# Kernel optimization log

Hardware: AMD Instinct MI355X
Metric: run time of the kernel (lower is better)

## Reference

```python
import jax, jax.numpy as jnp
import numpy as np

B, IN, N, OUT = 65536, 512, 256, 64  # batch, in_size, neurons, out_size


def setup_inputs() -> dict:
    key = jax.random.key(0)
    k1, k2, k3, k4 = jax.random.split(key, 4)
    return {
        "x": jax.random.normal(k1, (B, IN), jnp.float32),
        "W_lin": jax.random.normal(k2, (IN, N + OUT), jnp.float32),   # nlinear
        "W_nl": jax.random.normal(k3, (N - 1, N), jnp.float32),        # padded nonlinear[i] rows
        "W_out": jax.random.normal(k4, (OUT, N), jnp.float32),         # output_weights[0:out_size]
    }


def reference(x, W_lin, W_nl, W_out):
    act = jnp.tanh
    lin = x @ W_lin  # [B, N+OUT]
    # row i of nonlinear weights is valid only for entries 0..i (length i+1)
    tri_mask = (jnp.arange(N)[None, :] <= jnp.arange(N - 1)[:, None]).astype(lin.dtype)
    Wm = W_nl * tri_mask  # [N-1, N]
    # growing accumulator, fixed-size buffer; position 0 = lin[0] + 1
    acc0 = jnp.zeros((x.shape[0], N), lin.dtype).at[:, 0].set(lin[:, 0] + 1.0)
    col = jnp.arange(N)[None, :]

    def step(acc, inp):
        w, l, i = inp  # w: [N] masked weights, l: [B] = lin[:, i], i: scalar step
        v = jnp.sum(act(acc) * w[None, :], axis=1) + l + 1.0  # [B]
        acc = jnp.where(col == (i + 1), v[:, None], acc)
        return acc, None

    xs = (Wm, lin[:, : N - 1].T, jnp.arange(N - 1))
    acc, _ = jax.lax.scan(step, acc0, xs)
    # outs[i] = act(t) @ output_weights[i] + lin[neurons + i] + 1
    out = act(acc) @ W_out.T + lin[:, N:] + 1.0  # [B, OUT]
    return out
```

## Files before the change

### kernel.cpp

```cpp
#include <hip/hip_runtime.h>
#include <hip/hip_bf16.h>

typedef _Float16 f16x8 __attribute__((ext_vector_type(8)));
typedef unsigned short u16x8 __attribute__((ext_vector_type(8)));
typedef float f32x4 __attribute__((ext_vector_type(4)));
typedef unsigned int u32x4 __attribute__((ext_vector_type(4)));

static __device__ __forceinline__ unsigned short h2u(_Float16 h) {
    return __builtin_bit_cast(unsigned short, h);
}
static __device__ __forceinline__ float fast_tanh(float x) {
    float e = __expf(2.0f * x);
    return 1.0f - 2.0f / (e + 1.0f);
}

__global__ void cascade_prep(const float* __restrict__ W_lin,
                             const float* __restrict__ W_nl,
                             const float* __restrict__ W_out,
                             unsigned short* __restrict__ wlin_h,
                             unsigned short* __restrict__ wlin_l,
                             unsigned short* __restrict__ wnl_h,
                             unsigned short* __restrict__ wnl_l,
                             unsigned short* __restrict__ wout_h,
                             unsigned short* __restrict__ wout_l,
                             float* __restrict__ wcol) {
    int idx = blockIdx.x * blockDim.x + threadIdx.x;
    int stride = gridDim.x * blockDim.x;
    for (int i = idx; i < 320 * 512; i += stride) {
        int n = i >> 9, k = i & 511;
        float w = W_lin[k * 320 + n];
        _Float16 h = (_Float16)w;
        wlin_h[i] = h2u(h);
        wlin_l[i] = h2u((_Float16)(w - (float)h));
    }
    for (int i = idx; i < 255 * 256; i += stride) {
        int r = i >> 8, k = i & 255;
        float w = (k <= r) ? W_nl[i] : 0.0f;
        _Float16 h = (_Float16)w;
        wnl_h[i] = h2u(h);
        wnl_l[i] = h2u((_Float16)(w - (float)h));
    }
    for (int i = idx; i < 64 * 256; i += stride) {
        float w = W_out[i];
        _Float16 h = (_Float16)w;
        wout_h[i] = h2u(h);
        wout_l[i] = h2u((_Float16)(w - (float)h));
    }
    for (int i = idx; i < 256; i += stride) {
        int b = i >> 5, u = i & 31;
        float* dst = wcol + b * 496 + (31 * u - (u * (u - 1)) / 2);
        for (int j = u + 1; j < 32; ++j)
            dst[j - u - 1] = W_nl[(size_t)(b * 32 + j - 1) * 256 + b * 32 + u];
    }
}

__global__ __launch_bounds__(512, 1) void lin_gemm(
    const float* __restrict__ x,
    const unsigned short* __restrict__ wlin_h,
    const unsigned short* __restrict__ wlin_l,
    float* __restrict__ linc,
    float* __restrict__ lino) {

    __shared__ _Float16 bufH[2][16 * 520];
    __shared__ _Float16 bufL[2][16 * 520];

    const int tid = threadIdx.x;
    const int wv  = tid >> 6;
    const int l15 = tid & 15;
    const int g   = (tid & 63) >> 4;
    const int s = (blockIdx.x & 7) * 64 + (blockIdx.x >> 3);
    const long row0 = (long)s * 128;

    f16x8 xfh[16], xfl[16];
    {
        const float* xp = x + (row0 + wv * 16 + l15) * 512 + g * 8;
        #pragma unroll
        for (int ks = 0; ks < 16; ++ks) {
            float4 p0 = *reinterpret_cast<const float4*>(xp + ks * 32);
            float4 p1 = *reinterpret_cast<const float4*>(xp + ks * 32 + 4);
            float av[8] = {p0.x, p0.y, p0.z, p0.w, p1.x, p1.y, p1.z, p1.w};
            f16x8 fh, fl;
            #pragma unroll
            for (int e = 0; e < 8; ++e) {
                _Float16 hh = (_Float16)av[e];
                fh[e] = hh;
                fl[e] = (_Float16)(av[e] - (float)hh);
            }
            xfh[ks] = fh;
            xfl[ks] = fl;
        }
    }

    u16x8 rh[2], rl[2];
    #define STAGE_LOAD(nt)                                                     \
        {                                                                      \
            _Pragma("unroll")                                                  \
            for (int it = 0; it < 2; ++it) {                                   \
                int flat = it * 4096 + tid * 8;                                \
                int r = flat >> 9, c = flat & 511;                             \
                rh[it] = *reinterpret_cast<const u16x8*>(                      \
                    wlin_h + (size_t)((nt) * 16 + r) * 512 + c);               \
                rl[it] = *reinterpret_cast<const u16x8*>(                      \
                    wlin_l + (size_t)((nt) * 16 + r) * 512 + c);               \
            }                                                                  \
        }
    #define STAGE_WRITE(buf)                                                   \
        {                                                                      \
            _Pragma("unroll")                                                  \
            for (int it = 0; it < 2; ++it) {                                   \
                int flat = it * 4096 + tid * 8;                                \
                int r = flat >> 9, c = flat & 511;                             \
                *reinterpret_cast<u16x8*>(&bufH[buf][r * 520 + c]) =           \
                    __builtin_bit_cast(u16x8, rh[it]);                         \
                *reinterpret_cast<u16x8*>(&bufL[buf][r * 520 + c]) =           \
                    __builtin_bit_cast(u16x8, rl[it]);                         \
            }                                                                  \
        }

    STAGE_LOAD(0);
    STAGE_WRITE(0);
    __syncthreads();

    int cur = 0;
    for (int nt = 0; nt < 20; ++nt) {
        if (nt < 19) STAGE_LOAD(nt + 1);

        f32x4 acc = (f32x4){0.f, 0.f, 0.f, 0.f};
        if (nt < 16) {
            #pragma unroll
            for (int ks = 0; ks < 16; ++ks) {
                f16x8 bh = *reinterpret_cast<const f16x8*>(
                    &bufH[cur][l15 * 520 + ks * 32 + g * 8]);
                f16x8 bl = *reinterpret_cast<const f16x8*>(
                    &bufL[cur][l15 * 520 + ks * 32 + g * 8]);
                acc = __builtin_amdgcn_mfma_f32_16x16x32_f16(xfh[ks], bh, acc, 0, 0, 0);
                acc = __builtin_amdgcn_mfma_f32_16x16x32_f16(xfl[ks], bh, acc, 0, 0, 0);
                acc = __builtin_amdgcn_mfma_f32_16x16x32_f16(xfh[ks], bl, acc, 0, 0, 0);
            }
            int c = nt * 16 + l15;
            #pragma unroll
            for (int j = 0; j < 4; ++j) {
                long row = row0 + wv * 16 + g * 4 + j;
                if (c < 255) linc[row * 256 + c + 1] = acc[j];
                if (c == 0)  linc[row * 256] = acc[j];
            }
        } else {
            #pragma unroll
            for (int ks = 0; ks < 16; ++ks) {
                f16x8 bh = *reinterpret_cast<const f16x8*>(
                    &bufH[cur][l15 * 520 + ks * 32 + g * 8]);
                acc = __builtin_amdgcn_mfma_f32_16x16x32_f16(xfh[ks], bh, acc, 0, 0, 0);
            }
            #pragma unroll
            for (int j = 0; j < 4; ++j)
                lino[(row0 + wv * 16 + g * 4 + j) * 64 + (nt - 16) * 16 + l15] = acc[j];
        }

        if (nt < 19) STAGE_WRITE(cur ^ 1);
        __syncthreads();
        cur ^= 1;
    }
    #undef STAGE_LOAD
    #undef STAGE_WRITE
}

static __device__ __forceinline__ void unpack_pf(u32x4 a0, u32x4 a1,
                                                 f16x8* ah, f16x8* al) {
    u32x4 hx, lx;
    hx[0] = (a0[0] & 0xffffu) | (a0[1] << 16);
    hx[1] = (a0[2] & 0xffffu) | (a0[3] << 16);
    hx[2] = (a1[0] & 0xffffu) | (a1[1] << 16);
    hx[3] = (a1[2] & 0xffffu) | (a1[3] << 16);
    lx[0] = (a0[0] >> 16) | (a0[1] & 0xffff0000u);
    lx[1] = (a0[2] >> 16) | (a0[3] & 0xffff0000u);
    lx[2] = (a1[0] >> 16) | (a1[1] & 0xffff0000u);
    lx[3] = (a1[2] >> 16) | (a1[3] & 0xffff0000u);
    *ah = __builtin_bit_cast(f16x8, hx);
    *al = __builtin_bit_cast(f16x8, lx);
}

__global__ __launch_bounds__(64) void cascade_casc(
    const float* __restrict__ linc,
    const float* __restrict__ lino,
    const float* __restrict__ wcol,
    const unsigned short* __restrict__ wnl_h,
    const unsigned short* __restrict__ wnl_l,
    const unsigned short* __restrict__ wout_h,
    const unsigned short* __restrict__ wout_l,
    float* __restrict__ out) {

    __shared__ float conacc[32 * 260];
    __shared__ float wslab[500];

    const int l   = threadIdx.x;
    const int l15 = l & 15;
    const int g   = l >> 4;
    const int r   = l & 31;
    const int s = (blockIdx.x & 7) * 256 + (blockIdx.x >> 3);
    const long row0 = (long)s * 32;

    unsigned int* conp = reinterpret_cast<unsigned int*>(conacc);

    #pragma unroll
    for (int it = 0; it < 32; ++it) {
        int flat = it * 256 + l * 4;
        int rr = flat >> 8, c4 = flat & 255;
        float4 v = *reinterpret_cast<const float4*>(linc + (row0 + rr) * 256 + c4);
        *reinterpret_cast<float4*>(&conacc[rr * 260 + c4]) = v;
    }
    __syncthreads();

    for (int b = 0; b < 8; ++b) {
        {
            int i0 = l * 4;
            if (i0 < 496) {
                float4 v = *reinterpret_cast<const float4*>(wcol + b * 496 + i0);
                *reinterpret_cast<float4*>(&wslab[i0]) = v;
            }
            int i1 = 256 + l * 4;
            if (i1 < 496) {
                float4 v = *reinterpret_cast<const float4*>(wcol + b * 496 + i1);
                *reinterpret_cast<float4*>(&wslab[i1]) = v;
            }
        }
        __syncthreads();

        float acc[32];
        #pragma unroll
        for (int j = 0; j < 32; ++j) acc[j] = 0.0f;
        #pragma unroll
        for (int u8 = 0; u8 < 4; ++u8) {
            float4 cw0 = *reinterpret_cast<const float4*>(&conacc[r * 260 + b * 32 + u8 * 8]);
            float4 cw1 = *reinterpret_cast<const float4*>(&conacc[r * 260 + b * 32 + u8 * 8 + 4]);
            float conw[8] = {cw0.x, cw0.y, cw0.z, cw0.w, cw1.x, cw1.y, cw1.z, cw1.w};
            unsigned int pk[8];
            #pragma unroll
            for (int v = 0; v < 8; ++v) {
                const int u = u8 * 8 + v;
                float vv = acc[u] + conw[v] + 1.0f;
                float tv = fast_tanh(vv);
                _Float16 hv = (_Float16)tv;
                _Float16 lo = (_Float16)(tv - (float)hv);
                pk[v] = (unsigned int)h2u(hv) | ((unsigned int)h2u(lo) << 16);
                const float* wu = wslab + (31 * u - (u * (u - 1)) / 2);
                #pragma unroll
                for (int j = u + 1; j < 32; ++j)
                    acc[j] = fmaf(tv, wu[j - u - 1], acc[j]);
            }
            if (l < 32) {
                *reinterpret_cast<u32x4*>(&conp[r * 260 + b * 32 + u8 * 8]) =
                    (u32x4){pk[0], pk[1], pk[2], pk[3]};
                *reinterpret_cast<u32x4*>(&conp[r * 260 + b * 32 + u8 * 8 + 4]) =
                    (u32x4){pk[4], pk[5], pk[6], pk[7]};
            }
        }
        __syncthreads();

        if (b < 7) {
            f16x8 ah[2], al[2];
            #pragma unroll
            for (int m = 0; m < 2; ++m) {
                const unsigned int* p = &conp[(m * 16 + l15) * 260 + b * 32 + g * 8];
                unpack_pf(*reinterpret_cast<const u32x4*>(p),
                          *reinterpret_cast<const u32x4*>(p + 4), &ah[m], &al[m]);
            }
            for (int nt = 2 * (b + 1); nt < 16; ++nt) {
                const size_t wrow = (size_t)(nt * 16 + l15 - 1) * 256 + b * 32 + g * 8;
                f16x8 bh = __builtin_bit_cast(f16x8, *reinterpret_cast<const u16x8*>(wnl_h + wrow));
                f16x8 bl = __builtin_bit_cast(f16x8, *reinterpret_cast<const u16x8*>(wnl_l + wrow));
                #pragma unroll
                for (int m = 0; m < 2; ++m) {
                    f32x4 d = (f32x4){0.f, 0.f, 0.f, 0.f};
                    d = __builtin_amdgcn_mfma_f32_16x16x32_f16(ah[m], bh, d, 0, 0, 0);
                    d = __builtin_amdgcn_mfma_f32_16x16x32_f16(al[m], bh, d, 0, 0, 0);
                    d = __builtin_amdgcn_mfma_f32_16x16x32_f16(ah[m], bl, d, 0, 0, 0);
                    #pragma unroll
                    for (int jj = 0; jj < 4; ++jj) {
                        int idx = (m * 16 + g * 4 + jj) * 260 + nt * 16 + l15;
                        conacc[idx] += d[jj];
                    }
                }
            }
        }
        __syncthreads();
    }

    #pragma unroll
    for (int m = 0; m < 2; ++m) {
        #pragma unroll
        for (int n = 0; n < 4; ++n) {
            f32x4 acc = (f32x4){0.f, 0.f, 0.f, 0.f};
            #pragma unroll
            for (int kc = 0; kc < 8; ++kc) {
                const unsigned int* p = &conp[(m * 16 + l15) * 260 + kc * 32 + g * 8];
                f16x8 ah, al;
                unpack_pf(*reinterpret_cast<const u32x4*>(p),
                          *reinterpret_cast<const u32x4*>(p + 4), &ah, &al);
                const size_t wrow = (size_t)(n * 16 + l15) * 256 + kc * 32 + g * 8;
                f16x8 bh = __builtin_bit_cast(f16x8, *reinterpret_cast<const u16x8*>(wout_h + wrow));
                f16x8 bl = __builtin_bit_cast(f16x8, *reinterpret_cast<const u16x8*>(wout_l + wrow));
                acc = __builtin_amdgcn_mfma_f32_16x16x32_f16(ah, bh, acc, 0, 0, 0);
                acc = __builtin_amdgcn_mfma_f32_16x16x32_f16(al, bh, acc, 0, 0, 0);
                acc = __builtin_amdgcn_mfma_f32_16x16x32_f16(ah, bl, acc, 0, 0, 0);
            }
            #pragma unroll
            for (int j = 0; j < 4; ++j) {
                long rr = row0 + m * 16 + g * 4 + j;
                int c = n * 16 + l15;
                out[rr * 64 + c] = acc[j] + lino[rr * 64 + c] + 1.0f;
            }
        }
    }
}

extern "C" void kernel_launch(void* const* d_in, const int* in_sizes, int n_in,
                              void* d_out, int out_size, void* d_ws, size_t ws_size,
                              hipStream_t stream) {
    (void)in_sizes; (void)n_in; (void)out_size; (void)ws_size;
    const float* x     = (const float*)d_in[0];
    const float* W_lin = (const float*)d_in[1];
    const float* W_nl  = (const float*)d_in[2];
    const float* W_out = (const float*)d_in[3];
    float* out = (float*)d_out;

    char* ws = (char*)d_ws;
    unsigned short* wlin_h = (unsigned short*)(ws);
    unsigned short* wlin_l = (unsigned short*)(ws + 327680);
    unsigned short* wnl_h  = (unsigned short*)(ws + 916480);
    unsigned short* wnl_l  = (unsigned short*)(ws + 1047040);
    unsigned short* wout_h = (unsigned short*)(ws + 1177600);
    unsigned short* wout_l = (unsigned short*)(ws + 1210368);
    float*          wcol   = (float*)(ws + 1243136);
    float*          linc   = (float*)(ws + 1259008);
    float*          lino   = (float*)(ws + 68367872);

    cascade_prep<<<256, 256, 0, stream>>>(W_lin, W_nl, W_out,
                                          wlin_h, wlin_l, wnl_h, wnl_l,
                                          wout_h, wout_l, wcol);
    lin_gemm<<<512, 512, 0, stream>>>(x, wlin_h, wlin_l, linc, lino);
    cascade_casc<<<2048, 64, 0, stream>>>(linc, lino, wcol,
                                          wnl_h, wnl_l, wout_h, wout_l, out);
}
```

Measured before the change: 241.1 us.

## Split cascade block across four waves for MFMA update and output GEMM

Raises the cascade kernel block from one wave to four. The trailing MFMA updates of the accumulator are strided across waves, and each wave computes one output column tile. The serial tanh recurrence is executed redundantly by every wave with only the first wave storing results. The aim is more parallelism and latency hiding per LDS allocation, at the cost of duplicated scalar recurrence work and higher VALU contention.

Result: slower. 363.5 us (+50.8%).

```diff
diff --git a/kernel.cpp b/kernel.cpp
--- a/kernel.cpp
+++ b/kernel.cpp
@@ -179,7 +179,7 @@
     *al = __builtin_bit_cast(f16x8, lx);
 }
 
-__global__ __launch_bounds__(64) void cascade_casc(
+__global__ __launch_bounds__(256, 4) void cascade_casc(
     const float* __restrict__ linc,
     const float* __restrict__ lino,
     const float* __restrict__ wcol,
@@ -192,18 +192,19 @@
     __shared__ float conacc[32 * 260];
     __shared__ float wslab[500];
 
-    const int l   = threadIdx.x;
-    const int l15 = l & 15;
-    const int g   = l >> 4;
-    const int r   = l & 31;
+    const int tid = threadIdx.x;
+    const int wv  = tid >> 6;
+    const int l15 = tid & 15;
+    const int g   = (tid & 63) >> 4;
+    const int r   = tid & 31;
     const int s = (blockIdx.x & 7) * 256 + (blockIdx.x >> 3);
     const long row0 = (long)s * 32;
 
     unsigned int* conp = reinterpret_cast<unsigned int*>(conacc);
 
     #pragma unroll
-    for (int it = 0; it < 32; ++it) {
-        int flat = it * 256 + l * 4;
+    for (int it = 0; it < 8; ++it) {
+        int flat = it * 1024 + tid * 4;
         int rr = flat >> 8, c4 = flat & 255;
         float4 v = *reinterpret_cast<const float4*>(linc + (row0 + rr) * 256 + c4);
         *reinterpret_cast<float4*>(&conacc[rr * 260 + c4]) = v;
@@ -211,17 +212,9 @@
     __syncthreads();
 
     for (int b = 0; b < 8; ++b) {
-        {
-            int i0 = l * 4;
-            if (i0 < 496) {
-                float4 v = *reinterpret_cast<const float4*>(wcol + b * 496 + i0);
-                *reinterpret_cast<float4*>(&wslab[i0]) = v;
-            }
-            int i1 = 256 + l * 4;
-            if (i1 < 496) {
-                float4 v = *reinterpret_cast<const float4*>(wcol + b * 496 + i1);
-                *reinterpret_cast<float4*>(&wslab[i1]) = v;
-            }
+        if (tid * 4 < 496) {
+            float4 v = *reinterpret_cast<const float4*>(wcol + b * 496 + tid * 4);
+            *reinterpret_cast<float4*>(&wslab[tid * 4]) = v;
         }
         __syncthreads();
 
@@ -247,7 +240,7 @@
                 for (int j = u + 1; j < 32; ++j)
                     acc[j] = fmaf(tv, wu[j - u - 1], acc[j]);
             }
-            if (l < 32) {
+            if (tid < 32) {
                 *reinterpret_cast<u32x4*>(&conp[r * 260 + b * 32 + u8 * 8]) =
                     (u32x4){pk[0], pk[1], pk[2], pk[3]};
                 *reinterpret_cast<u32x4*>(&conp[r * 260 + b * 32 + u8 * 8 + 4]) =
@@ -264,7 +257,7 @@
                 unpack_pf(*reinterpret_cast<const u32x4*>(p),
                           *reinterpret_cast<const u32x4*>(p + 4), &ah[m], &al[m]);
             }
-            for (int nt = 2 * (b + 1); nt < 16; ++nt) {
+            for (int nt = 2 * (b + 1) + wv; nt < 16; nt += 4) {
                 const size_t wrow = (size_t)(nt * 16 + l15 - 1) * 256 + b * 32 + g * 8;
                 f16x8 bh = __builtin_bit_cast(f16x8, *reinterpret_cast<const u16x8*>(wnl_h + wrow));
                 f16x8 bl = __builtin_bit_cast(f16x8, *reinterpret_cast<const u16x8*>(wnl_l + wrow));
@@ -285,10 +278,10 @@
         __syncthreads();
     }
 
-    #pragma unroll
-    for (int m = 0; m < 2; ++m) {
+    {
+        const int n = wv;
         #pragma unroll
-        for (int n = 0; n < 4; ++n) {
+        for (int m = 0; m < 2; ++m) {
             f32x4 acc = (f32x4){0.f, 0.f, 0.f, 0.f};
             #pragma unroll
             for (int kc = 0; kc < 8; ++kc) {
@@ -338,6 +331,6 @@
                                           wlin_h, wlin_l, wnl_h, wnl_l,
                                           wout_h, wout_l, wcol);
     lin_gemm<<<512, 512, 0, stream>>>(x, wlin_h, wlin_l, linc, lino);
-    cascade_casc<<<2048, 64, 0, stream>>>(linc, lino, wcol,
-                                          wnl_h, wnl_l, wout_h, wout_l, out);
-}
+    cascade_casc<<<2048, 256, 0, stream>>>(linc, lino, wcol,
+                                           wnl_h, wnl_l, wout_h, wout_l, out);
+}
```
